# Optimization experiments

Measured on AMD Instinct MI355X. Metric: run time of the kernel, lower is better.

Reference implementation:

```python
import jax, jax.numpy as jnp
import numpy as np

N, E, H = 16384, 32768, 64          # nodes, edges, res_h_edge
M0, M1 = 32, 8                      # res_irreps = 32x0e + 8x1o
RES_DIM = M0 + 3 * M1               # 56
TP_IN0, TP_IN1 = 2 * M0, 2 * M1     # tp_in_irreps = 64x0e + 16x1o
W_IN = TP_IN0 + TP_IN1              # 80 (fan-in of the '0e' weight path)
W_NUMEL = W_IN * H


def setup_inputs() -> dict:
    key = jax.random.key(0)
    ks = jax.random.split(key, 8)
    res_features = jax.random.normal(ks[0], (N, RES_DIM), jnp.float32)
    edge_features = jax.random.normal(ks[1], (E, H), jnp.float32)
    edge_sh = jax.random.normal(ks[2], (E, 4), jnp.float32)
    edge_index = jax.random.randint(ks[3], (2, E), 0, N, dtype=jnp.int64)
    # FFN params: Linear(H, 2H) -> ReLU -> Linear(2H, W_NUMEL)
    W1 = jax.random.normal(ks[4], (H, 2 * H), jnp.float32) / np.sqrt(H).astype(np.float32)
    b1 = jnp.zeros((2 * H,), jnp.float32)
    W2 = jax.random.normal(ks[5], (2 * H, W_NUMEL), jnp.float32) / np.sqrt(2 * H).astype(np.float32)
    b2 = jnp.zeros((W_NUMEL,), jnp.float32)
    # LayerNorm affine params
    gamma = jnp.ones((H,), jnp.float32)
    beta = jnp.zeros((H,), jnp.float32)
    return dict(res_features=res_features, edge_features=edge_features,
                edge_sh=edge_sh, W1=W1, b1=b1, W2=W2, b2=b2,
                gamma=gamma, beta=beta, edge_index=edge_index)


def reference(res_features, edge_features, edge_sh, W1, b1, W2, b2, gamma, beta, edge_index):
    # gather endpoint features per edge
    src = res_features[edge_index[1]]   # [E, 56]
    dst = res_features[edge_index[0]]   # [E, 56]
    E_ = src.shape[0]
    # tp_input layout per original cat: [src_0e, dst_0e, src_1o, dst_1o]
    s = jnp.concatenate([src[:, :M0], dst[:, :M0]], axis=-1)               # [E, 64] scalars (0e)
    v = jnp.concatenate([src[:, M0:].reshape(E_, M1, 3),
                         dst[:, M0:].reshape(E_, M1, 3)], axis=1)          # [E, 16, 3] vectors (1o)
    # spherical harmonics 1x0e+1x1o
    sh0 = edge_sh[:, 0]                                                    # [E]
    sh1 = edge_sh[:, 1:4]                                                  # [E, 3]
    # 0e x 0e -> 0e and 1o . 1o / sqrt(3) -> 0e
    feat0 = s * sh0[:, None]                                               # [E, 64]
    feat1 = jnp.einsum('evn,en->ev', v, sh1) / np.float32(np.sqrt(3.0))    # [E, 16]
    feats = jnp.concatenate([feat0, feat1], axis=-1)                       # [E, 80]
    # per-edge weights generated by FFN, normalized by sqrt(fan_in)
    w = jax.nn.relu(edge_features @ W1 + b1) @ W2 + b2                      # [E, 5120]
    w = w.reshape(E_, W_IN, H) / np.float32(np.sqrt(W_IN))                  # [E, 80, 64]
    tp_update = jnp.einsum('ed,edh->eh', feats, w)                          # [E, 64]
    # residual + LayerNorm
    x = edge_features + tp_update
    mu = jnp.mean(x, axis=-1, keepdims=True)
    var = jnp.var(x, axis=-1, keepdims=True)
    return (x - mu) * jax.lax.rsqrt(var + np.float32(1e-5)) * gamma + beta
```

## Files before the change

### kernel.cpp

```cpp
#include <hip/hip_runtime.h>
#include <hip/hip_bf16.h>


using short8   = __attribute__((ext_vector_type(8))) short;
using floatx16 = __attribute__((ext_vector_type(16))) float;

constexpr int NE = 32768;

constexpr size_t W2A_OFF = 0;
constexpr size_t B2A_OFF = 0x140000;
constexpr size_t W1P_OFF = 0x144000;

__device__ __forceinline__ float bfbits2f(short s) {
  unsigned u = ((unsigned)(unsigned short)s) << 16;
  return __builtin_bit_cast(float, u);
}
__device__ __forceinline__ short f2bfbits(float f) {
  __hip_bfloat16 h = __float2bfloat16(f);
  return __builtin_bit_cast(short, h);
}
__device__ __forceinline__ bool is_bf16_mode(const void* gamma) {
  return *(const unsigned*)gamma == 0x3F803F80u;
}
__device__ __forceinline__ float loadf(const void* p, long i, bool isbf) {
  return isbf ? bfbits2f(((const short*)p)[i]) : ((const float*)p)[i];
}

__global__ void pack_kernel(const void* __restrict__ W2, const void* __restrict__ b2,
                            const void* __restrict__ W1, const void* __restrict__ gamma,
                            short* __restrict__ w2a, short* __restrict__ b2a,
                            short* __restrict__ w1p) {
  const bool isbf = is_bf16_mode(gamma);
  int i = blockIdx.x * 256 + threadIdx.x;
  if (i < 81920) {
    int l = i & 63, s = (i >> 6) & 7, c = i >> 9;
    int d = c >> 1, p = c & 1;
    int dh = d * 64 + p * 32 + (l & 31);
    int kb = s * 16 + (l >> 5) * 8;
    short8 o;
#pragma unroll
    for (int j = 0; j < 8; ++j) o[j] = f2bfbits(loadf(W2, (long)(kb + j) * 5120 + dh, isbf));
    *(short8*)(w2a + (long)i * 8) = o;
  } else if (i < 82560) {
    int i2 = i - 81920;
    int l = i2 & 63, s = (i2 >> 6) % 5, p = i2 / 320;
    int kb = s * 16 + (l >> 5) * 8;
    int h = p * 32 + (l & 31);
    short8 o;
#pragma unroll
    for (int j = 0; j < 8; ++j) o[j] = f2bfbits(loadf(b2, (long)(kb + j) * 64 + h, isbf));
    *(short8*)(b2a + (long)i2 * 8) = o;
  } else if (i < 83584) {
    int i3 = i - 82560;
    int l = i3 & 63, g = i3 >> 6;
    int s = g >> 2, t = g & 3;
    int kb = s * 16 + (l >> 5) * 8, n = t * 32 + (l & 31);
    short8 o;
#pragma unroll
    for (int j = 0; j < 8; ++j) o[j] = f2bfbits(loadf(W1, (long)(kb + j) * 128 + n, isbf));
    *(short8*)(w1p + (long)i3 * 8) = o;
  }
}

__global__ __launch_bounds__(256, 3)
void fused_kernel(const void* __restrict__ res, const void* __restrict__ sh,
                  const void* __restrict__ idxp, const void* __restrict__ ef,
                  const void* __restrict__ b1, const void* __restrict__ gamma,
                  const void* __restrict__ beta, const short* __restrict__ w2a,
                  const short* __restrict__ b2a, const short* __restrict__ w1p,
                  void* __restrict__ out) {
  const bool isbf = is_bf16_mode(gamma);
  __shared__ int h1t_i[64 * 68];
  __shared__ float ftf[64 * 81];
  __shared__ int sflag;
  short* h1t = (short*)h1t_i;
  float* xsum = (float*)h1t_i;

  const int tid = threadIdx.x;
  const int l = tid & 63, w = tid >> 6;
  const int lane31 = l & 31, half = l >> 5;
  const int e0 = blockIdx.x * 64;

  if (tid == 0) {
    const int* ip = (const int*)idxp;
    int nz = 0;
    for (int i = 0; i < 64; ++i) nz |= ip[2 * i + 1];
    sflag = (nz == 0) ? 1 : 0;
  }
  __syncthreads();
  const bool is64 = (sflag != 0);

  {
    const float inv80 = 0.11180339887498949f;
    int el = tid >> 2, q = tid & 3, e = e0 + el;
    long row;
    if (is64) {
      const long long* lp = (const long long*)idxp;
      row = (long)((q < 2) ? lp[NE + e] : lp[e]);
    } else {
      const int* ip = (const int*)idxp;
      row = (q < 2) ? ip[NE + e] : ip[e];
    }
    float sh0 = loadf(sh, (long)e * 4 + 0, isbf) * inv80;
    float s1x = loadf(sh, (long)e * 4 + 1, isbf);
    float s1y = loadf(sh, (long)e * 4 + 2, isbf);
    float s1z = loadf(sh, (long)e * 4 + 3, isbf);
    const int part = q & 1;

    float vals[16];
    if (isbf) {
      const short* rp = (const short*)res + row * 56 + part * 16;
      short8 v0 = *(const short8*)rp;
      short8 v1 = *(const short8*)(rp + 8);
#pragma unroll
      for (int j = 0; j < 8; ++j) { vals[j] = bfbits2f(v0[j]) * sh0; vals[8 + j] = bfbits2f(v1[j]) * sh0; }
    } else {
      const float* rp = (const float*)res + row * 56 + part * 16;
#pragma unroll
      for (int j = 0; j < 16; ++j) vals[j] = rp[j] * sh0;
    }
    int abase = (q < 2 ? 0 : 32) + part * 16;
    float* fo = ftf + el * 81 + abase;
#pragma unroll
    for (int j = 0; j < 16; ++j) fo[j] = vals[j];

    if (part) {
      float r24[24];
      if (isbf) {
        const short* rp = (const short*)res + row * 56 + 32;
#pragma unroll
        for (int c = 0; c < 3; ++c) {
          short8 v = *(const short8*)(rp + c * 8);
#pragma unroll
          for (int j = 0; j < 8; ++j) r24[c * 8 + j] = bfbits2f(v[j]);
        }
      } else {
        const float* rp = (const float*)res + row * 56 + 32;
#pragma unroll
        for (int j = 0; j < 24; ++j) r24[j] = rp[j];
      }
      const float c3 = 0.57735026918962576f * inv80;
      float* vo = ftf + el * 81 + 64 + (q < 2 ? 0 : 8);
#pragma unroll
      for (int j = 0; j < 8; ++j)
        vo[j] = (r24[3 * j] * s1x + r24[3 * j + 1] * s1y + r24[3 * j + 2] * s1z) * c3;
    }
  }

  {
    int mt = w >> 1, ntp = w & 1;
    int erow = e0 + mt * 32 + lane31;
    floatx16 acc2[2];
#pragma unroll
    for (int t = 0; t < 2; ++t)
#pragma unroll
      for (int i = 0; i < 16; ++i) acc2[t][i] = 0.f;
    const short8* wp = (const short8*)w1p;
#pragma unroll
    for (int s2 = 0; s2 < 4; ++s2) {
      short8 a;
      if (isbf) {
        a = *(const short8*)((const short*)ef + (long)erow * 64 + s2 * 16 + half * 8);
      } else {
        const float* fp = (const float*)ef + (long)erow * 64 + s2 * 16 + half * 8;
#pragma unroll
        for (int j = 0; j < 8; ++j) a[j] = f2bfbits(fp[j]);
      }
      short8 bA = wp[(s2 * 4 + ntp * 2 + 0) * 64 + l];
      short8 bB = wp[(s2 * 4 + ntp * 2 + 1) * 64 + l];
      acc2[0] = __builtin_amdgcn_mfma_f32_32x32x16_bf16(a, bA, acc2[0], 0, 0, 0);
      acc2[1] = __builtin_amdgcn_mfma_f32_32x32x16_bf16(a, bB, acc2[1], 0, 0, 0);
    }
#pragma unroll
    for (int t = 0; t < 2; ++t) {
      int col = (ntp * 2 + t) * 32 + lane31;
      float bias = loadf(b1, col, isbf);
#pragma unroll
      for (int r = 0; r < 16; ++r) {
        int rrow = (r & 3) + 8 * (r >> 2) + 4 * half;
        float v = acc2[t][r] + bias;
        v = v > 0.f ? v : 0.f;
        h1t[(mt * 32 + rrow) * 136 + col] = f2bfbits(v);
      }
    }
  }
  __syncthreads();

  const int ks = w & 1, p = w >> 1;
  short8 B0[4], B1[4];
#pragma unroll
  for (int s2 = 0; s2 < 4; ++s2) {
    B0[s2] = *(const short8*)(h1t + lane31 * 136 + ks * 64 + s2 * 16 + half * 8);
    B1[s2] = *(const short8*)(h1t + (32 + lane31) * 136 + ks * 64 + s2 * 16 + half * 8);
  }
  __syncthreads();

  {
    int el = tid >> 2, q = tid & 3;
    float v[16];
    if (isbf) {
      const short* ep = (const short*)ef + (long)(e0 + el) * 64 + q * 16;
      short8 v0 = *(const short8*)ep;
      short8 v1 = *(const short8*)(ep + 8);
#pragma unroll
      for (int j = 0; j < 8; ++j) { v[j] = bfbits2f(v0[j]); v[8 + j] = bfbits2f(v1[j]); }
    } else {
      const float* ep = (const float*)ef + (long)(e0 + el) * 64 + q * 16;
#pragma unroll
      for (int j = 0; j < 16; ++j) v[j] = ep[j];
    }
    float* xp = xsum + el * 65 + q * 16;
#pragma unroll
    for (int j = 0; j < 16; ++j) xp[j] = v[j];
  }
  __syncthreads();

  const float* frow0 = ftf + lane31 * 81;
  const float* frow1 = ftf + (32 + lane31) * 81;
  floatx16 wacc0, wacc1, tpl0, tpl1;
#pragma unroll
  for (int i = 0; i < 16; ++i) { wacc0[i] = 0.f; wacc1[i] = 0.f; tpl0[i] = 0.f; tpl1[i] = 0.f; }

  const short8* ap = (const short8*)w2a + (p * 8 + ks * 4) * 64 + l;
  short8 A[4];
#pragma unroll
  for (int s2 = 0; s2 < 4; ++s2) A[s2] = ap[s2 * 64];
  float fc0 = frow0[0], fc1 = frow1[0];

  for (int dd = 0; dd < 79; ++dd) {
    const short8* apn = ap + 1024;
    short8 An0 = apn[0], An1 = apn[64], An2 = apn[128], An3 = apn[192];
    float fn0 = frow0[dd + 1], fn1 = frow1[dd + 1];

    wacc0 = __builtin_amdgcn_mfma_f32_32x32x16_bf16(A[0], B0[0], wacc0, 0, 0, 0);
    wacc1 = __builtin_amdgcn_mfma_f32_32x32x16_bf16(A[0], B1[0], wacc1, 0, 0, 0);
    wacc0 = __builtin_amdgcn_mfma_f32_32x32x16_bf16(A[1], B0[1], wacc0, 0, 0, 0);
    wacc1 = __builtin_amdgcn_mfma_f32_32x32x16_bf16(A[1], B1[1], wacc1, 0, 0, 0);
    wacc0 = __builtin_amdgcn_mfma_f32_32x32x16_bf16(A[2], B0[2], wacc0, 0, 0, 0);
    wacc1 = __builtin_amdgcn_mfma_f32_32x32x16_bf16(A[2], B1[2], wacc1, 0, 0, 0);
    wacc0 = __builtin_amdgcn_mfma_f32_32x32x16_bf16(A[3], B0[3], wacc0, 0, 0, 0);
    wacc1 = __builtin_amdgcn_mfma_f32_32x32x16_bf16(A[3], B1[3], wacc1, 0, 0, 0);

    float c0 = fc0 - fn0, c1 = fc1 - fn1;
#pragma unroll
    for (int r = 0; r < 16; ++r) {
      tpl0[r] = fmaf(c0, wacc0[r], tpl0[r]);
      tpl1[r] = fmaf(c1, wacc1[r], tpl1[r]);
    }
    A[0] = An0; A[1] = An1; A[2] = An2; A[3] = An3;
    fc0 = fn0; fc1 = fn1;
    ap = apn;
  }
  {
    wacc0 = __builtin_amdgcn_mfma_f32_32x32x16_bf16(A[0], B0[0], wacc0, 0, 0, 0);
    wacc1 = __builtin_amdgcn_mfma_f32_32x32x16_bf16(A[0], B1[0], wacc1, 0, 0, 0);
    wacc0 = __builtin_amdgcn_mfma_f32_32x32x16_bf16(A[1], B0[1], wacc0, 0, 0, 0);
    wacc1 = __builtin_amdgcn_mfma_f32_32x32x16_bf16(A[1], B1[1], wacc1, 0, 0, 0);
    wacc0 = __builtin_amdgcn_mfma_f32_32x32x16_bf16(A[2], B0[2], wacc0, 0, 0, 0);
    wacc1 = __builtin_amdgcn_mfma_f32_32x32x16_bf16(A[2], B1[2], wacc1, 0, 0, 0);
    wacc0 = __builtin_amdgcn_mfma_f32_32x32x16_bf16(A[3], B0[3], wacc0, 0, 0, 0);
    wacc1 = __builtin_amdgcn_mfma_f32_32x32x16_bf16(A[3], B1[3], wacc1, 0, 0, 0);
#pragma unroll
    for (int r = 0; r < 16; ++r) {
      tpl0[r] = fmaf(fc0, wacc0[r], tpl0[r]);
      tpl1[r] = fmaf(fc1, wacc1[r], tpl1[r]);
    }
  }

#pragma unroll
  for (int r = 0; r < 16; ++r) {
    int hrow = p * 32 + (r & 3) + 8 * (r >> 2) + 4 * half;
    atomicAdd(xsum + lane31 * 65 + hrow, tpl0[r]);
    atomicAdd(xsum + (32 + lane31) * 65 + hrow, tpl1[r]);
  }

  if (ks == 0) {
    floatx16 bacc0, bacc1;
#pragma unroll
    for (int i = 0; i < 16; ++i) { bacc0[i] = 0.f; bacc1[i] = 0.f; }
#pragma unroll
    for (int s2 = 0; s2 < 5; ++s2) {
      short8 bfA = *((const short8*)b2a + (p * 5 + s2) * 64 + l);
      short8 fb0, fb1;
#pragma unroll
      for (int j = 0; j < 8; ++j) {
        fb0[j] = f2bfbits(frow0[s2 * 16 + half * 8 + j]);
        fb1[j] = f2bfbits(frow1[s2 * 16 + half * 8 + j]);
      }
      bacc0 = __builtin_amdgcn_mfma_f32_32x32x16_bf16(bfA, fb0, bacc0, 0, 0, 0);
      bacc1 = __builtin_amdgcn_mfma_f32_32x32x16_bf16(bfA, fb1, bacc1, 0, 0, 0);
    }
#pragma unroll
    for (int r = 0; r < 16; ++r) {
      int hrow = p * 32 + (r & 3) + 8 * (r >> 2) + 4 * half;
      atomicAdd(xsum + lane31 * 65 + hrow, bacc0[r]);
      atomicAdd(xsum + (32 + lane31) * 65 + hrow, bacc1[r]);
    }
  }
  __syncthreads();

  {
    int el = tid >> 2, q = tid & 3;
    const float* xr = xsum + el * 65 + q * 16;
    float x[16], sm = 0.f, ssm = 0.f;
#pragma unroll
    for (int i = 0; i < 16; ++i) { x[i] = xr[i]; sm += x[i]; ssm += x[i] * x[i]; }
    sm += __shfl_xor(sm, 1);  ssm += __shfl_xor(ssm, 1);
    sm += __shfl_xor(sm, 2);  ssm += __shfl_xor(ssm, 2);
    float mu = sm * 0.015625f;
    float var = ssm * 0.015625f - mu * mu;
    float rstd = rsqrtf(var + 1e-5f);
    long ob = (long)(e0 + el) * 64 + q * 16;
    if (isbf) {
      short8 o0, o1;
#pragma unroll
      for (int i = 0; i < 8; ++i) {
        int c0 = q * 16 + i, c1 = q * 16 + 8 + i;
        float g0 = bfbits2f(((const short*)gamma)[c0]), b0 = bfbits2f(((const short*)beta)[c0]);
        float g1 = bfbits2f(((const short*)gamma)[c1]), b1v = bfbits2f(((const short*)beta)[c1]);
        o0[i] = f2bfbits((x[i] - mu) * rstd * g0 + b0);
        o1[i] = f2bfbits((x[8 + i] - mu) * rstd * g1 + b1v);
      }
      *(short8*)((short*)out + ob) = o0;
      *(short8*)((short*)out + ob + 8) = o1;
    } else {
      float* op = (float*)out + ob;
#pragma unroll
      for (int i = 0; i < 16; ++i) {
        int c = q * 16 + i;
        op[i] = (x[i] - mu) * rstd * ((const float*)gamma)[c] + ((const float*)beta)[c];
      }
    }
  }
}

extern "C" void kernel_launch(void* const* d_in, const int* in_sizes, int n_in,
                              void* d_out, int out_size, void* d_ws, size_t ws_size,
                              hipStream_t stream) {
  const void* res   = d_in[0];
  const void* ef    = d_in[1];
  const void* sh    = d_in[2];
  const void* W1    = d_in[3];
  const void* b1    = d_in[4];
  const void* W2    = d_in[5];
  const void* b2    = d_in[6];
  const void* gamma = d_in[7];
  const void* beta  = d_in[8];
  const void* idx   = d_in[9];

  char* ws = (char*)d_ws;
  short* w2a = (short*)(ws + W2A_OFF);
  short* b2a = (short*)(ws + B2A_OFF);
  short* w1p = (short*)(ws + W1P_OFF);

  pack_kernel<<<(83584 + 255) / 256, 256, 0, stream>>>(W2, b2, W1, gamma, w2a, b2a, w1p);
  fused_kernel<<<NE / 64, 256, 0, stream>>>(res, sh, idx, ef, b1, gamma, beta,
                                            w2a, b2a, w1p, d_out);
}
```

Before: 163.8 us.

## Split tensor-product reduction across two blocks per edge tile with separate LayerNorm kernel

Each 64-edge tile is now processed by two blocks, each covering half of the 80-wide fan-in dimension. Each block writes a partial fp32 sum to a workspace buffer, and a new ln_kernel adds the residual and both partials before applying LayerNorm. This doubles the grid to improve occupancy and parallelism across CUs. In exchange, each block redoes the gather and the first FFN layer, the partials make an extra global round trip, and there is one more kernel launch.

```diff
diff --git a/kernel.cpp b/kernel.cpp
--- a/kernel.cpp
+++ b/kernel.cpp
@@ -7,9 +7,11 @@
 
 constexpr int NE = 32768;
 
-constexpr size_t W2A_OFF = 0;
-constexpr size_t B2A_OFF = 0x140000;
-constexpr size_t W1P_OFF = 0x144000;
+constexpr size_t W2A_OFF   = 0;
+constexpr size_t B2A_OFF   = 0x140000;
+constexpr size_t W1P_OFF   = 0x144000;
+constexpr size_t PBUFA_OFF = 0x180000;
+constexpr size_t PBUFB_OFF = 0x980000;
 
 __device__ __forceinline__ float bfbits2f(short s) {
   unsigned u = ((unsigned)(unsigned short)s) << 16;
@@ -66,9 +68,9 @@
 void fused_kernel(const void* __restrict__ res, const void* __restrict__ sh,
                   const void* __restrict__ idxp, const void* __restrict__ ef,
                   const void* __restrict__ b1, const void* __restrict__ gamma,
-                  const void* __restrict__ beta, const short* __restrict__ w2a,
-                  const short* __restrict__ b2a, const short* __restrict__ w1p,
-                  void* __restrict__ out) {
+                  const short* __restrict__ w2a, const short* __restrict__ b2a,
+                  const short* __restrict__ w1p,
+                  float* __restrict__ pbufA, float* __restrict__ pbufB) {
   const bool isbf = is_bf16_mode(gamma);
   __shared__ int h1t_i[64 * 68];
   __shared__ float ftf[64 * 81];
@@ -79,7 +81,9 @@
   const int tid = threadIdx.x;
   const int l = tid & 63, w = tid >> 6;
   const int lane31 = l & 31, half = l >> 5;
-  const int e0 = blockIdx.x * 64;
+  const int bid = blockIdx.x;
+  const int dh2 = bid & 1;
+  const int e0 = (bid >> 1) * 64;
 
   if (tid == 0) {
     const int* ip = (const int*)idxp;
@@ -195,39 +199,23 @@
   }
   __syncthreads();
 
-  {
-    int el = tid >> 2, q = tid & 3;
-    float v[16];
-    if (isbf) {
-      const short* ep = (const short*)ef + (long)(e0 + el) * 64 + q * 16;
-      short8 v0 = *(const short8*)ep;
-      short8 v1 = *(const short8*)(ep + 8);
-#pragma unroll
-      for (int j = 0; j < 8; ++j) { v[j] = bfbits2f(v0[j]); v[8 + j] = bfbits2f(v1[j]); }
-    } else {
-      const float* ep = (const float*)ef + (long)(e0 + el) * 64 + q * 16;
-#pragma unroll
-      for (int j = 0; j < 16; ++j) v[j] = ep[j];
-    }
-    float* xp = xsum + el * 65 + q * 16;
-#pragma unroll
-    for (int j = 0; j < 16; ++j) xp[j] = v[j];
-  }
-  __syncthreads();
-
-  const float* frow0 = ftf + lane31 * 81;
-  const float* frow1 = ftf + (32 + lane31) * 81;
+  for (int i = tid; i < 64 * 65; i += 256) xsum[i] = 0.f;
+  __syncthreads();
+
+  const int dlo = dh2 * 40;
+  const float* frow0 = ftf + lane31 * 81 + dlo;
+  const float* frow1 = ftf + (32 + lane31) * 81 + dlo;
   floatx16 wacc0, wacc1, tpl0, tpl1;
 #pragma unroll
   for (int i = 0; i < 16; ++i) { wacc0[i] = 0.f; wacc1[i] = 0.f; tpl0[i] = 0.f; tpl1[i] = 0.f; }
 
-  const short8* ap = (const short8*)w2a + (p * 8 + ks * 4) * 64 + l;
+  const short8* ap = (const short8*)w2a + ((dlo * 2 + p) * 8 + ks * 4) * 64 + l;
   short8 A[4];
 #pragma unroll
   for (int s2 = 0; s2 < 4; ++s2) A[s2] = ap[s2 * 64];
   float fc0 = frow0[0], fc1 = frow1[0];
 
-  for (int dd = 0; dd < 79; ++dd) {
+  for (int dd = 0; dd < 39; ++dd) {
     const short8* apn = ap + 1024;
     short8 An0 = apn[0], An1 = apn[64], An2 = apn[128], An3 = apn[192];
     float fn0 = frow0[dd + 1], fn1 = frow1[dd + 1];
@@ -274,18 +262,20 @@
     atomicAdd(xsum + (32 + lane31) * 65 + hrow, tpl1[r]);
   }
 
-  if (ks == 0) {
+  if (dh2 == 0 && ks == 0) {
     floatx16 bacc0, bacc1;
 #pragma unroll
     for (int i = 0; i < 16; ++i) { bacc0[i] = 0.f; bacc1[i] = 0.f; }
+    const float* f0 = ftf + lane31 * 81;
+    const float* f1 = ftf + (32 + lane31) * 81;
 #pragma unroll
     for (int s2 = 0; s2 < 5; ++s2) {
       short8 bfA = *((const short8*)b2a + (p * 5 + s2) * 64 + l);
       short8 fb0, fb1;
 #pragma unroll
       for (int j = 0; j < 8; ++j) {
-        fb0[j] = f2bfbits(frow0[s2 * 16 + half * 8 + j]);
-        fb1[j] = f2bfbits(frow1[s2 * 16 + half * 8 + j]);
+        fb0[j] = f2bfbits(f0[s2 * 16 + half * 8 + j]);
+        fb1[j] = f2bfbits(f1[s2 * 16 + half * 8 + j]);
       }
       bacc0 = __builtin_amdgcn_mfma_f32_32x32x16_bf16(bfA, fb0, bacc0, 0, 0, 0);
       bacc1 = __builtin_amdgcn_mfma_f32_32x32x16_bf16(bfA, fb1, bacc1, 0, 0, 0);
@@ -300,36 +290,73 @@
   __syncthreads();
 
   {
+    float* slice = (dh2 ? pbufB : pbufA) + (long)e0 * 64;
     int el = tid >> 2, q = tid & 3;
     const float* xr = xsum + el * 65 + q * 16;
-    float x[16], sm = 0.f, ssm = 0.f;
-#pragma unroll
-    for (int i = 0; i < 16; ++i) { x[i] = xr[i]; sm += x[i]; ssm += x[i] * x[i]; }
-    sm += __shfl_xor(sm, 1);  ssm += __shfl_xor(ssm, 1);
-    sm += __shfl_xor(sm, 2);  ssm += __shfl_xor(ssm, 2);
-    float mu = sm * 0.015625f;
-    float var = ssm * 0.015625f - mu * mu;
-    float rstd = rsqrtf(var + 1e-5f);
-    long ob = (long)(e0 + el) * 64 + q * 16;
+    float* op = slice + el * 64 + q * 16;
+#pragma unroll
+    for (int i = 0; i < 4; ++i) {
+      float4 v = { xr[i * 4], xr[i * 4 + 1], xr[i * 4 + 2], xr[i * 4 + 3] };
+      *(float4*)(op + i * 4) = v;
+    }
+  }
+}
+
+__global__ __launch_bounds__(256, 8)
+void ln_kernel(const void* __restrict__ ef, const void* __restrict__ gamma,
+               const void* __restrict__ beta, const float* __restrict__ pbufA,
+               const float* __restrict__ pbufB, void* __restrict__ out) {
+  const bool isbf = is_bf16_mode(gamma);
+  const int tid = threadIdx.x;
+  const int el = tid >> 2, q = tid & 3;
+  const long e = (long)blockIdx.x * 64 + el;
+  const long base = e * 64 + q * 16;
+
+  float x[16], sm = 0.f, ssm = 0.f;
+#pragma unroll
+  for (int i = 0; i < 4; ++i) {
+    float4 a = *(const float4*)(pbufA + base + i * 4);
+    float4 b = *(const float4*)(pbufB + base + i * 4);
+    float ev[4];
     if (isbf) {
-      short8 o0, o1;
-#pragma unroll
-      for (int i = 0; i < 8; ++i) {
-        int c0 = q * 16 + i, c1 = q * 16 + 8 + i;
-        float g0 = bfbits2f(((const short*)gamma)[c0]), b0 = bfbits2f(((const short*)beta)[c0]);
-        float g1 = bfbits2f(((const short*)gamma)[c1]), b1v = bfbits2f(((const short*)beta)[c1]);
-        o0[i] = f2bfbits((x[i] - mu) * rstd * g0 + b0);
-        o1[i] = f2bfbits((x[8 + i] - mu) * rstd * g1 + b1v);
-      }
-      *(short8*)((short*)out + ob) = o0;
-      *(short8*)((short*)out + ob + 8) = o1;
+      ushort4 u = *(const ushort4*)((const ushort*)ef + base + i * 4);
+      ev[0] = bfbits2f((short)u.x); ev[1] = bfbits2f((short)u.y);
+      ev[2] = bfbits2f((short)u.z); ev[3] = bfbits2f((short)u.w);
     } else {
-      float* op = (float*)out + ob;
-#pragma unroll
-      for (int i = 0; i < 16; ++i) {
-        int c = q * 16 + i;
-        op[i] = (x[i] - mu) * rstd * ((const float*)gamma)[c] + ((const float*)beta)[c];
-      }
+      float4 u = *(const float4*)((const float*)ef + base + i * 4);
+      ev[0] = u.x; ev[1] = u.y; ev[2] = u.z; ev[3] = u.w;
+    }
+    const float* ax = &a.x; const float* bx = &b.x;
+#pragma unroll
+    for (int j = 0; j < 4; ++j) {
+      float v = ev[j] + ax[j] + bx[j];
+      x[i * 4 + j] = v; sm += v; ssm += v * v;
+    }
+  }
+  sm += __shfl_xor(sm, 1);  ssm += __shfl_xor(ssm, 1);
+  sm += __shfl_xor(sm, 2);  ssm += __shfl_xor(ssm, 2);
+  float mu = sm * 0.015625f;
+  float var = ssm * 0.015625f - mu * mu;
+  float rstd = rsqrtf(var + 1e-5f);
+
+  if (isbf) {
+    short8 o0, o1;
+#pragma unroll
+    for (int i = 0; i < 8; ++i) {
+      int c0 = q * 16 + i, c1 = q * 16 + 8 + i;
+      float g0 = bfbits2f(((const short*)gamma)[c0]), b0 = bfbits2f(((const short*)beta)[c0]);
+      float g1 = bfbits2f(((const short*)gamma)[c1]), b1 = bfbits2f(((const short*)beta)[c1]);
+      o0[i] = f2bfbits((x[i] - mu) * rstd * g0 + b0);
+      o1[i] = f2bfbits((x[8 + i] - mu) * rstd * g1 + b1);
+    }
+    *(short8*)((short*)out + base) = o0;
+    *(short8*)((short*)out + base + 8) = o1;
+  } else {
+    float* op = (float*)out + base;
+#pragma unroll
+    for (int i = 0; i < 16; ++i) {
+      int c = q * 16 + i;
+      op[i] = (x[i] - mu) * rstd * ((const float*)gamma)[c] + ((const float*)beta)[c];
     }
   }
 }
@@ -349,11 +376,14 @@
   const void* idx   = d_in[9];
 
   char* ws = (char*)d_ws;
-  short* w2a = (short*)(ws + W2A_OFF);
-  short* b2a = (short*)(ws + B2A_OFF);
-  short* w1p = (short*)(ws + W1P_OFF);
+  short* w2a   = (short*)(ws + W2A_OFF);
+  short* b2a   = (short*)(ws + B2A_OFF);
+  short* w1p   = (short*)(ws + W1P_OFF);
+  float* pbufA = (float*)(ws + PBUFA_OFF);
+  float* pbufB = (float*)(ws + PBUFB_OFF);
 
   pack_kernel<<<(83584 + 255) / 256, 256, 0, stream>>>(W2, b2, W1, gamma, w2a, b2a, w1p);
-  fused_kernel<<<NE / 64, 256, 0, stream>>>(res, sh, idx, ef, b1, gamma, beta,
-                                            w2a, b2a, w1p, d_out);
-}
+  fused_kernel<<<NE / 64 * 2, 256, 0, stream>>>(res, sh, idx, ef, b1, gamma,
+                                                w2a, b2a, w1p, pbufA, pbufB);
+  ln_kernel<<<NE / 64, 256, 0, stream>>>(ef, gamma, beta, pbufA, pbufB, d_out);
+}
```

Result: slower. 199.6 us (+21.9%).
